# Kernel tuning notes

Measured on AMD Instinct MI355X. Metric: run time of the kernel, lower is better.

Reference implementation:

```python
import jax, jax.numpy as jnp
import numpy as np

H, DH, DM = 8, 128, 1024          # n_head, d_head, d_model (n_head*d_head == d_model)
SLEN, BSZ = 256, 64               # slen <= 256 forced by pi0[:, :l]
SCALE = 1.0 / DH ** 0.5
LN_EPS = 1e-5


def setup_inputs() -> dict:
    key = jax.random.key(0)
    k0, k1, k2, k3 = jax.random.split(key, 4)
    h = jax.random.normal(k0, (SLEN, BSZ, DM), jnp.float32)
    W_qkv = jax.random.normal(k1, (H * 4 * DH, DM), jnp.float32) * (DM ** -0.5)
    W_o = jax.random.normal(k2, (DM, H * DH), jnp.float32) * ((H * DH) ** -0.5)
    pi0 = jax.random.uniform(k3, (H, 256), jnp.float32)
    ln_gamma = jnp.ones((DM,), jnp.float32)
    ln_beta = jnp.zeros((DM,), jnp.float32)
    return {"h": h, "W_qkv": W_qkv, "W_o": W_o, "pi0": pi0,
            "ln_gamma": ln_gamma, "ln_beta": ln_beta}


def _phi(x):
    # elu(x)+1 feature map, then L1-normalize over the feature dim
    x = jax.nn.elu(x) + 1.0
    return x / jnp.sum(x, axis=-1, keepdims=True)


def _causal_linear_attn(q, k, v):
    # fast_weight_sum: out_t = sum_{s<=t} (q_t . k_s) v_s  (zero initial fast weights)
    # q,k,v: [b,h,l,d]
    l = q.shape[2]
    scores = jnp.einsum('bhld,bhsd->bhls', q, k)
    mask = jnp.tril(jnp.ones((l, l), dtype=bool))
    scores = jnp.where(mask, scores, jnp.zeros((), scores.dtype))
    return jnp.einsum('bhls,bhsd->bhld', scores, v)


def reference(h, W_qkv, W_o, pi0, ln_gamma, ln_beta):
    l, b, _ = h.shape
    # qkv projection: [l,b,H,4*DH] -> q, k1, k2, v (update_mode='rbf2keys')
    qkv = jnp.einsum('lbm,nm->lbn', h, W_qkv).reshape(l, b, H, 4 * DH)
    q, k1, k2, v = jnp.split(qkv, 4, axis=-1)
    # permute to [b, H, l, d]
    q = _phi(jnp.transpose(q, (1, 2, 0, 3)))
    k1 = _phi(jnp.transpose(k1, (1, 2, 0, 3)))
    k2 = _phi(jnp.transpose(k2, (1, 2, 0, 3)))
    v = jnp.transpose(v, (1, 2, 0, 3))
    # two fast-weight sums (skip_attn_normalization=True path)
    lo1 = _causal_linear_attn(q, k1, v)
    lo2 = _causal_linear_attn(q, k2, v)
    pi = jnp.clip(pi0, 0.0, 1.0)[None, :, :l, None]          # [1,H,l,1]
    layer_out = SCALE * (lo1 * pi + lo2 * (1.0 - pi))         # [b,H,l,d]
    # [b,H,l,d] -> [l,b,H*d]
    layer_out = jnp.transpose(layer_out, (2, 0, 1, 3)).reshape(l, b, H * DH)
    attn_out = jnp.einsum('lbn,mn->lbm', layer_out, W_o)
    # post-LN residual (pre_lnorm=False, dropout=0)
    x = h + attn_out
    mu = jnp.mean(x, axis=-1, keepdims=True)
    var = jnp.mean((x - mu) ** 2, axis=-1, keepdims=True)
    return ln_gamma * (x - mu) / jnp.sqrt(var + LN_EPS) + ln_beta
```

## Files before the change

### kernel.cpp

```cpp
#include <hip/hip_runtime.h>

#define H_     8
#define DM_    1024
#define NQKV_  4096
#define ROWS_  16384
#define PAIRS_ 512
#define SCALE_ 0.08838834764831845f
#define LN_EPS_ 1e-5f

typedef __attribute__((ext_vector_type(8))) short short8;
typedef __attribute__((ext_vector_type(4))) short short4v;
typedef __attribute__((ext_vector_type(4))) float floatx4;

__device__ __forceinline__ float b2f(unsigned short u) {
  union { unsigned int i; float f; } v; v.i = ((unsigned int)u) << 16; return v.f;
}
__device__ __forceinline__ unsigned short f2b(float f) {
  union { unsigned int i; float f; } v; v.f = f;
  unsigned int b = v.i;
  b += 0x7FFFu + ((b >> 16) & 1u);
  return (unsigned short)(b >> 16);
}

__device__ __forceinline__ void stage_async(const unsigned short* __restrict__ g,
                                            size_t ld, unsigned short* s, int tid) {
#pragma unroll
  for (int p = 0; p < 4; ++p) {
    int idx = p * 256 + tid;
    int r = idx >> 3, j = idx & 7;
    int cg = j ^ (r & 7);
    __builtin_amdgcn_global_load_lds(
        (const __attribute__((address_space(1))) unsigned int*)(g + (size_t)r * ld + cg * 8),
        (__attribute__((address_space(3))) unsigned int*)(s + (size_t)idx * 8),
        16, 0, 0);
  }
}
__device__ __forceinline__ void stage_h(const unsigned short* __restrict__ g,
                                        size_t o0, size_t o1,
                                        unsigned short* s, int lo0, int lo1) {
  __builtin_amdgcn_global_load_lds(
      (const __attribute__((address_space(1))) unsigned int*)(g + o0),
      (__attribute__((address_space(3))) unsigned int*)(s + lo0), 16, 0, 0);
  __builtin_amdgcn_global_load_lds(
      (const __attribute__((address_space(1))) unsigned int*)(g + o1),
      (__attribute__((address_space(3))) unsigned int*)(s + lo1), 16, 0, 0);
}
__device__ __forceinline__ short8 lds_frag(const unsigned short* s, int row, int cg) {
  return *(const short8*)(s + row * 64 + ((cg ^ (row & 7)) << 3));
}

__global__ __launch_bounds__(256) void cvt_all(const float* __restrict__ h,
                                               const float* __restrict__ wq,
                                               const float* __restrict__ wo,
                                               unsigned short* __restrict__ hb,
                                               unsigned short* __restrict__ wqb,
                                               unsigned short* __restrict__ wob) {
  int i = blockIdx.x * 256 + threadIdx.x;
  const float* src; unsigned short* dst; int off;
  if (i < 2097152)      { src = h;  dst = hb;  off = i; }
  else if (i < 2621440) { src = wq; dst = wqb; off = i - 2097152; }
  else                  { src = wo; dst = wob; off = i - 2621440; }
  const float4* s4 = (const float4*)(src + (size_t)off * 8);
  float4 v0 = s4[0], v1 = s4[1];
  union { short8 v; unsigned short u[8]; } pk;
  pk.u[0] = f2b(v0.x); pk.u[1] = f2b(v0.y); pk.u[2] = f2b(v0.z); pk.u[3] = f2b(v0.w);
  pk.u[4] = f2b(v1.x); pk.u[5] = f2b(v1.y); pk.u[6] = f2b(v1.z); pk.u[7] = f2b(v1.w);
  *(short8*)(dst + (size_t)off * 8) = pk.v;
}

#define TILE_BODY(T, BUF, OBUF)                                                \
  {                                                                            \
    unsigned short* SB = (BUF) + 16384;                                        \
    const unsigned short* aA0 = (BUF) + (wm * 128 + l16) * 64 + ((quad ^ s7) << 3); \
    const unsigned short* aA1 = (BUF) + (wm * 128 + l16) * 64 + (((4 + quad) ^ s7) << 3); \
    const unsigned short* bA0 = SB + (wn * 64 + l16) * 64 + ((quad ^ s7) << 3);\
    const unsigned short* bA1 = SB + (wn * 64 + l16) * 64 + (((4 + quad) ^ s7) << 3); \
    short8 a[8], b[4];                                                         \
                   \
    if ((T) < 15) {                                                            \
      size_t kn = (size_t)((T) + 1) * 64;                                      \
      stage_h(BbP + kn,  oB0, oB1, (OBUF) + 16384, lo0, lo1);                  \
      stage_h(BbHP + kn, oB0, oB1, (OBUF) + 24576, lo0, lo1);                  \
    }                                                                          \
    _Pragma("unroll")                                                          \
    for (int mt = 0; mt < 4; ++mt) {                                           \
      a[mt * 2 + 0] = *(const short8*)(aA0 + mt * 1024);                       \
      a[mt * 2 + 1] = *(const short8*)(aA1 + mt * 1024);                       \
    }                                                                          \
    _Pragma("unroll")                                                          \
    for (int nt = 0; nt < 2; ++nt) {                                           \
      b[nt * 2 + 0] = *(const short8*)(bA0 + nt * 1024);                       \
      b[nt * 2 + 1] = *(const short8*)(bA1 + nt * 1024);                       \
    }                                                                          \
    __builtin_amdgcn_sched_barrier(0);                                         \
    __builtin_amdgcn_s_barrier();                                              \
    __builtin_amdgcn_s_setprio(1);                                             \
    _Pragma("unroll")                                                          \
    for (int kk = 0; kk < 2; ++kk)                                             \
      _Pragma("unroll")                                                        \
      for (int m = 0; m < 4; ++m)                                              \
        _Pragma("unroll")                                                      \
        for (int n = 0; n < 2; ++n)                                            \
          acc[m][n] = __builtin_amdgcn_mfma_f32_16x16x32_bf16(a[m * 2 + kk], b[n * 2 + kk], acc[m][n], 0, 0, 0); \
    __builtin_amdgcn_s_setprio(0);                                             \
    __builtin_amdgcn_s_barrier();                                              \
                                                 \
    _Pragma("unroll")                                                          \
    for (int nt = 0; nt < 2; ++nt) {                                           \
      b[nt * 2 + 0] = *(const short8*)(bA0 + 2048 + nt * 1024);                \
      b[nt * 2 + 1] = *(const short8*)(bA1 + 2048 + nt * 1024);                \
    }                                                                          \
    __builtin_amdgcn_sched_barrier(0);                                         \
    __builtin_amdgcn_s_barrier();                                              \
    __builtin_amdgcn_s_setprio(1);                                             \
    _Pragma("unroll")                                                          \
    for (int kk = 0; kk < 2; ++kk)                                             \
      _Pragma("unroll")                                                        \
      for (int m = 0; m < 4; ++m)                                              \
        _Pragma("unroll")                                                      \
        for (int n = 0; n < 2; ++n)                                            \
          acc[m][2 + n] = __builtin_amdgcn_mfma_f32_16x16x32_bf16(a[m * 2 + kk], b[n * 2 + kk], acc[m][2 + n], 0, 0, 0); \
    __builtin_amdgcn_s_setprio(0);                                             \
    __builtin_amdgcn_s_barrier();                                              \
                                       \
    _Pragma("unroll")                                                          \
    for (int mt = 0; mt < 4; ++mt) {                                           \
      a[mt * 2 + 0] = *(const short8*)(aA0 + 4096 + mt * 1024);                \
      a[mt * 2 + 1] = *(const short8*)(aA1 + 4096 + mt * 1024);                \
    }                                                                          \
    __builtin_amdgcn_sched_barrier(0);                                         \
    __builtin_amdgcn_s_barrier();                                              \
    __builtin_amdgcn_s_setprio(1);                                             \
    _Pragma("unroll")                                                          \
    for (int kk = 0; kk < 2; ++kk)                                             \
      _Pragma("unroll")                                                        \
      for (int m = 0; m < 4; ++m)                                              \
        _Pragma("unroll")                                                      \
        for (int n = 0; n < 2; ++n)                                            \
          acc[4 + m][2 + n] = __builtin_amdgcn_mfma_f32_16x16x32_bf16(a[m * 2 + kk], b[n * 2 + kk], acc[4 + m][2 + n], 0, 0, 0); \
    __builtin_amdgcn_s_setprio(0);                                             \
    __builtin_amdgcn_s_barrier();                                              \
                \
    if ((T) < 14) {                                                            \
      size_t kt2 = (size_t)((T) + 2) * 64;                                     \
      stage_h(AbP + kt2,  oA0, oA1, (BUF),        lo0, lo1);                   \
      stage_h(AbHP + kt2, oA0, oA1, (BUF) + 8192, lo0, lo1);                   \
    }                                                                          \
    _Pragma("unroll")                                                          \
    for (int nt = 0; nt < 2; ++nt) {                                           \
      b[nt * 2 + 0] = *(const short8*)(bA0 + nt * 1024);                       \
      b[nt * 2 + 1] = *(const short8*)(bA1 + nt * 1024);                       \
    }                                                                          \
    __builtin_amdgcn_sched_barrier(0);                                         \
    __builtin_amdgcn_s_barrier();                                              \
    __builtin_amdgcn_s_setprio(1);                                             \
    _Pragma("unroll")                                                          \
    for (int kk = 0; kk < 2; ++kk)                                             \
      _Pragma("unroll")                                                        \
      for (int m = 0; m < 4; ++m)                                              \
        _Pragma("unroll")                                                      \
        for (int n = 0; n < 2; ++n)                                            \
          acc[4 + m][n] = __builtin_amdgcn_mfma_f32_16x16x32_bf16(a[m * 2 + kk], b[n * 2 + kk], acc[4 + m][n], 0, 0, 0); \
    __builtin_amdgcn_s_setprio(0);                                             \
    if ((T) < 14) { asm volatile("s_waitcnt vmcnt(4)" ::: "memory"); }         \
    else          { asm volatile("s_waitcnt vmcnt(0)" ::: "memory"); }         \
    __builtin_amdgcn_s_barrier();                                              \
  }

__global__ __launch_bounds__(512, 1) void qkv_gemm(const unsigned short* __restrict__ A,
                                                   const unsigned short* __restrict__ B,
                                                   unsigned short* __restrict__ QKV) {
  __shared__ alignas(16) unsigned short Sh[65536];
  int tid = threadIdx.x;
  int lane = tid & 63, wid = tid >> 6;
  int wm = wid >> 2, wn = wid & 3;
  int quad = lane >> 4, l16 = lane & 15;
  int s7 = l16 & 7;

  int bid = blockIdx.y * 16 + blockIdx.x;
  int swz = (bid & 7) * 128 + (bid >> 3);
  int bx = swz & 15, by = swz >> 4;
  int n0 = bx * 256, hh = bx >> 1, part0 = (bx & 1) * 2, bb = by;

  const unsigned short* AbP = A + (size_t)bb * DM_;
  const size_t lda = (size_t)64 * DM_;
  const unsigned short* AbHP = AbP + (size_t)128 * lda;
  const unsigned short* BbP = B + (size_t)n0 * DM_;
  const unsigned short* BbHP = BbP + (size_t)128 * DM_;

  int r0 = tid >> 3, jj = tid & 7;
  int cg = jj ^ (r0 & 7);
  size_t oA0 = (size_t)r0 * lda + cg * 8;
  size_t oA1 = (size_t)(r0 + 64) * lda + cg * 8;
  size_t oB0 = (size_t)r0 * DM_ + cg * 8;
  size_t oB1 = (size_t)(r0 + 64) * DM_ + cg * 8;
  int lo0 = tid * 8, lo1 = 4096 + tid * 8;

  floatx4 acc[8][4];
#pragma unroll
  for (int i = 0; i < 8; ++i)
#pragma unroll
    for (int j = 0; j < 4; ++j)
#pragma unroll
      for (int r = 0; r < 4; ++r) acc[i][j][r] = 0.f;

  stage_h(AbP,        oA0, oA1, Sh,         lo0, lo1);
  stage_h(AbHP,       oA0, oA1, Sh + 8192,  lo0, lo1);
  stage_h(BbP,        oB0, oB1, Sh + 16384, lo0, lo1);
  stage_h(BbHP,       oB0, oB1, Sh + 24576, lo0, lo1);
  stage_h(AbP + 64,   oA0, oA1, Sh + 32768, lo0, lo1);
  stage_h(AbHP + 64,  oA0, oA1, Sh + 40960, lo0, lo1);
  asm volatile("s_waitcnt vmcnt(4)" ::: "memory");
  __builtin_amdgcn_s_barrier();

  for (int t = 0; t < 16; t += 2) {
    TILE_BODY(t,     Sh,         Sh + 32768)
    TILE_BODY(t + 1, Sh + 32768, Sh)
  }

  __syncthreads();
  bool isV = (part0 + (wn >> 1)) == 3;
  float* Pf = (float*)Sh;
  float rsum[8][4];
  float inv[8][4];
  if (!isV) {
#pragma unroll
    for (int mt = 0; mt < 8; ++mt)
#pragma unroll
      for (int r = 0; r < 4; ++r) rsum[mt][r] = 0.f;
#pragma unroll
    for (int mt = 0; mt < 8; ++mt)
#pragma unroll
      for (int nt = 0; nt < 4; ++nt)
#pragma unroll
        for (int r = 0; r < 4; ++r) {
          float x = acc[mt][nt][r];
          float f = x > 0.f ? x + 1.f : __expf(x);
          acc[mt][nt][r] = f;
          rsum[mt][r] += f;
        }
#pragma unroll
    for (int off = 1; off < 16; off <<= 1)
#pragma unroll
      for (int mt = 0; mt < 8; ++mt)
#pragma unroll
        for (int r = 0; r < 4; ++r)
          rsum[mt][r] += __shfl_xor(rsum[mt][r], off);
    if (l16 == 0) {
#pragma unroll
      for (int mt = 0; mt < 8; ++mt)
#pragma unroll
        for (int r = 0; r < 4; ++r)
          Pf[(wm * 128 + mt * 16 + quad * 4 + r) * 4 + wn] = rsum[mt][r];
    }
  }
  __syncthreads();
  if (!isV) {
#pragma unroll
    for (int mt = 0; mt < 8; ++mt)
#pragma unroll
      for (int r = 0; r < 4; ++r)
        inv[mt][r] = 1.f / (rsum[mt][r] + Pf[(wm * 128 + mt * 16 + quad * 4 + r) * 4 + (wn ^ 1)]);
  }
  __syncthreads();

#pragma unroll
  for (int hq = 0; hq < 2; ++hq) {
    int part = part0 + hq;
    if ((wn >> 1) == hq) {
      if (part < 3) {
#pragma unroll
        for (int mt = 0; mt < 8; ++mt)
#pragma unroll
          for (int nt = 0; nt < 4; ++nt)
#pragma unroll
            for (int r = 0; r < 4; ++r) {
              int row = wm * 128 + mt * 16 + quad * 4 + r;
              int col = (wn & 1) * 64 + nt * 16 + l16;
              Sh[row * 136 + col] = f2b(acc[mt][nt][r] * inv[mt][r]);
            }
      } else {
#pragma unroll
        for (int mt = 0; mt < 8; ++mt)
#pragma unroll
          for (int nt = 0; nt < 4; ++nt)
#pragma unroll
            for (int r = 0; r < 4; ++r) {
              int d = (wn & 1) * 64 + nt * 16 + l16;
              int l = wm * 128 + mt * 16 + quad * 4 + r;
              Sh[d * 264 + l] = f2b(acc[mt][nt][r]);
            }
      }
    }
    __syncthreads();
    if (part < 3) {
      unsigned short* P = QKV + (size_t)part * 16777216 + (size_t)(bb * 8 + hh) * 32768;
      int c = tid & 15, g = tid >> 4;
#pragma unroll
      for (int j = 0; j < 8; ++j) {
        int row = j * 32 + g;
        *(short8*)(P + (size_t)row * 128 + c * 8) = *(const short8*)(Sh + row * 136 + c * 8);
      }
    } else {
      unsigned short* Vt = QKV + (size_t)3 * 16777216 + (size_t)(bb * 8 + hh) * 32768;
      int cg2 = tid & 31, g = tid >> 5;
#pragma unroll
      for (int j = 0; j < 8; ++j) {
        int d = j * 16 + g;
        *(short8*)(Vt + (size_t)d * 256 + cg2 * 8) = *(const short8*)(Sh + d * 264 + cg2 * 8);
      }
    }
    __syncthreads();
  }
}

__global__ __launch_bounds__(256) void scores_kernel(const unsigned short* __restrict__ QKV,
                                                     const float* __restrict__ pi0,
                                                     unsigned short* __restrict__ S) {
  __shared__ alignas(16) unsigned short Sh[24576];
  __shared__ float pis[128];
  unsigned short* As  = Sh;
  unsigned short* Bs1 = Sh + 8192;
  unsigned short* Bs2 = Sh + 16384;
  int p = blockIdx.z;
  int hh = p & 7;
  int tid = threadIdx.x;
  int lane = tid & 63, wid = tid >> 6;
  int wm = wid >> 1, wn = wid & 1;
  int quad = lane >> 4, l16 = lane & 15;
  int tix = blockIdx.x;
  int m0 = (tix >= 1) ? 128 : 0;
  int n0 = (tix == 2) ? 128 : 0;
  if (tid < 128) {
    float pv = pi0[hh * 256 + m0 + tid];
    pis[tid] = fminf(fmaxf(pv, 0.f), 1.f);
  }
  const unsigned short* Qb  = QKV + (size_t)p * 32768 + (size_t)m0 * 128;
  const unsigned short* K1b = QKV + 16777216     + (size_t)p * 32768 + (size_t)n0 * 128;
  const unsigned short* K2b = QKV + 2 * 16777216 + (size_t)p * 32768 + (size_t)n0 * 128;

  floatx4 acc1[4][4], acc2[4][4];
#pragma unroll
  for (int i = 0; i < 4; ++i)
#pragma unroll
    for (int j = 0; j < 4; ++j)
#pragma unroll
      for (int r = 0; r < 4; ++r) { acc1[i][j][r] = 0.f; acc2[i][j][r] = 0.f; }

  for (int kt = 0; kt < 128; kt += 64) {
    stage_async(Qb + kt, 128, As, tid);
    stage_async(K1b + kt, 128, Bs1, tid);
    stage_async(K2b + kt, 128, Bs2, tid);
    __syncthreads();
#pragma unroll
    for (int kk = 0; kk < 2; ++kk) {
      short8 af[4], b1[4], b2v[4];
#pragma unroll
      for (int mt = 0; mt < 4; ++mt)
        af[mt] = lds_frag(As, wm * 64 + mt * 16 + l16, kk * 4 + quad);
#pragma unroll
      for (int nt = 0; nt < 4; ++nt) {
        b1[nt]  = lds_frag(Bs1, wn * 64 + nt * 16 + l16, kk * 4 + quad);
        b2v[nt] = lds_frag(Bs2, wn * 64 + nt * 16 + l16, kk * 4 + quad);
      }
#pragma unroll
      for (int mt = 0; mt < 4; ++mt)
#pragma unroll
        for (int nt = 0; nt < 4; ++nt) {
          acc1[mt][nt] = __builtin_amdgcn_mfma_f32_16x16x32_bf16(af[mt], b1[nt],  acc1[mt][nt], 0, 0, 0);
          acc2[mt][nt] = __builtin_amdgcn_mfma_f32_16x16x32_bf16(af[mt], b2v[nt], acc2[mt][nt], 0, 0, 0);
        }
    }
    __syncthreads();
  }
#pragma unroll
  for (int mt = 0; mt < 4; ++mt)
#pragma unroll
    for (int nt = 0; nt < 4; ++nt)
#pragma unroll
      for (int r = 0; r < 4; ++r) {
        int tl = wm * 64 + mt * 16 + quad * 4 + r;
        int sl = wn * 64 + nt * 16 + l16;
        float pv = pis[tl];
        float v = (n0 + sl <= m0 + tl) ? (pv * acc1[mt][nt][r] + (1.f - pv) * acc2[mt][nt][r]) : 0.f;
        Sh[tl * 136 + sl] = f2b(v);
      }
  __syncthreads();
  int c = tid & 15, g = tid >> 4;
#pragma unroll
  for (int j = 0; j < 8; ++j) {
    int r = j * 16 + g;
    size_t gb = (size_t)p * 65536 + (size_t)(m0 + r) * 256 + n0 + c * 8;
    *(short8*)(S + gb) = *(const short8*)(Sh + r * 136 + c * 8);
  }
}

__global__ __launch_bounds__(256, 4) void pv_kernel(const unsigned short* __restrict__ S,
                                                    const unsigned short* __restrict__ Vt,
                                                    unsigned short* __restrict__ LO) {
  __shared__ alignas(16) unsigned short Sh[17408];
  unsigned short* As = Sh;
  unsigned short* Bs = Sh + 8192;
  int p = blockIdx.z;
  int b = p >> 3, hh = p & 7;
  int tid = threadIdx.x;
  int lane = tid & 63, wid = tid >> 6;
  int wm = wid >> 1, wn = wid & 1;
  int quad = lane >> 4, l16 = lane & 15;
  int m0 = blockIdx.y * 128;
  int kEnd = (blockIdx.y == 0) ? 128 : 256;
  const unsigned short* Ab = S  + (size_t)p * 65536 + (size_t)m0 * 256;
  const unsigned short* Bb = Vt + (size_t)p * 32768;

  floatx4 acc[4][4];
#pragma unroll
  for (int i = 0; i < 4; ++i)
#pragma unroll
    for (int j = 0; j < 4; ++j)
#pragma unroll
      for (int r = 0; r < 4; ++r) acc[i][j][r] = 0.f;

  for (int kt = 0; kt < kEnd; kt += 64) {
    stage_async(Ab + kt, 256, As, tid);
    stage_async(Bb + kt, 256, Bs, tid);
    __syncthreads();
#pragma unroll
    for (int kk = 0; kk < 2; ++kk) {
      short8 af[4], bfv[4];
#pragma unroll
      for (int mt = 0; mt < 4; ++mt)
        af[mt] = lds_frag(As, wm * 64 + mt * 16 + l16, kk * 4 + quad);
#pragma unroll
      for (int nt = 0; nt < 4; ++nt)
        bfv[nt] = lds_frag(Bs, wn * 64 + nt * 16 + l16, kk * 4 + quad);
#pragma unroll
      for (int mt = 0; mt < 4; ++mt)
#pragma unroll
        for (int nt = 0; nt < 4; ++nt)
          acc[mt][nt] = __builtin_amdgcn_mfma_f32_16x16x32_bf16(af[mt], bfv[nt], acc[mt][nt], 0, 0, 0);
    }
    __syncthreads();
  }
#pragma unroll
  for (int mt = 0; mt < 4; ++mt)
#pragma unroll
    for (int nt = 0; nt < 4; ++nt)
#pragma unroll
      for (int r = 0; r < 4; ++r) {
        int tl = wm * 64 + mt * 16 + quad * 4 + r;
        int d = wn * 64 + nt * 16 + l16;
        Sh[tl * 136 + d] = f2b(SCALE_ * acc[mt][nt][r]);
      }
  __syncthreads();
  int c = tid & 15, g = tid >> 4;
#pragma unroll
  for (int j = 0; j < 8; ++j) {
    int r = j * 16 + g;
    int t = m0 + r;
    size_t gb = ((size_t)t * 64 + b) * 1024 + hh * 128 + c * 8;
    *(short8*)(LO + gb) = *(const short8*)(Sh + r * 136 + c * 8);
  }
}

__global__ __launch_bounds__(512, 1) void wo_gemm(const unsigned short* __restrict__ A,
                                                  const unsigned short* __restrict__ B,
                                                  unsigned short* __restrict__ attn) {
  __shared__ alignas(16) unsigned short Sh[65536];
  int tid = threadIdx.x;
  int lane = tid & 63, wid = tid >> 6;
  int wm = wid >> 2, wn = wid & 3;
  int quad = lane >> 4, l16 = lane & 15;
  int s7 = l16 & 7;

  int bid = blockIdx.y * 4 + blockIdx.x;
  int swz = (bid & 7) * 32 + (bid >> 3);
  int bx = swz & 3, by = swz >> 2;
  int n0 = bx * 256, m0 = by * 256;

  const unsigned short* AbP = A + (size_t)m0 * DM_;
  const unsigned short* AbHP = AbP + (size_t)128 * DM_;
  const unsigned short* BbP = B + (size_t)n0 * DM_;
  const unsigned short* BbHP = BbP + (size_t)128 * DM_;

  int r0 = tid >> 3, jj = tid & 7;
  int cg = jj ^ (r0 & 7);
  size_t oA0 = (size_t)r0 * DM_ + cg * 8;
  size_t oA1 = (size_t)(r0 + 64) * DM_ + cg * 8;
  size_t oB0 = oA0, oB1 = oA1;
  int lo0 = tid * 8, lo1 = 4096 + tid * 8;

  floatx4 acc[8][4];
#pragma unroll
  for (int i = 0; i < 8; ++i)
#pragma unroll
    for (int j = 0; j < 4; ++j)
#pragma unroll
      for (int r = 0; r < 4; ++r) acc[i][j][r] = 0.f;

  stage_h(AbP,        oA0, oA1, Sh,         lo0, lo1);
  stage_h(AbHP,       oA0, oA1, Sh + 8192,  lo0, lo1);
  stage_h(BbP,        oB0, oB1, Sh + 16384, lo0, lo1);
  stage_h(BbHP,       oB0, oB1, Sh + 24576, lo0, lo1);
  stage_h(AbP + 64,   oA0, oA1, Sh + 32768, lo0, lo1);
  stage_h(AbHP + 64,  oA0, oA1, Sh + 40960, lo0, lo1);
  asm volatile("s_waitcnt vmcnt(4)" ::: "memory");
  __builtin_amdgcn_s_barrier();

  for (int t = 0; t < 16; t += 2) {
    TILE_BODY(t,     Sh,         Sh + 32768)
    TILE_BODY(t + 1, Sh + 32768, Sh)
  }

  __syncthreads();
#pragma unroll
  for (int hq = 0; hq < 2; ++hq) {
    if ((wn >> 1) == hq) {
#pragma unroll
      for (int mt = 0; mt < 8; ++mt)
#pragma unroll
        for (int nt = 0; nt < 4; ++nt)
#pragma unroll
          for (int r = 0; r < 4; ++r) {
            int row = wm * 128 + mt * 16 + quad * 4 + r;
            int col = (wn & 1) * 64 + nt * 16 + l16;
            Sh[row * 136 + col] = f2b(acc[mt][nt][r]);
          }
    }
    __syncthreads();
    int c = tid & 15, g = tid >> 4;
#pragma unroll
    for (int j = 0; j < 8; ++j) {
      int row = j * 32 + g;
      *(short8*)(attn + (size_t)(m0 + row) * DM_ + n0 + hq * 128 + c * 8) =
          *(const short8*)(Sh + row * 136 + c * 8);
    }
    __syncthreads();
  }
}

__global__ __launch_bounds__(256) void ln_res(const unsigned short* __restrict__ attn,
                                              const float* __restrict__ hin,
                                              const float* __restrict__ gamma,
                                              const float* __restrict__ beta,
                                              float* __restrict__ out) {
  int row = blockIdx.x;
  int tid = threadIdx.x;
  const unsigned short* ap = attn + (size_t)row * DM_ + tid * 4;
  const float* hp = hin + (size_t)row * DM_ + tid * 4;
  short4v av = *(const short4v*)ap;
  float4 hv = *(const float4*)hp;
  float x[4];
  x[0] = hv.x + b2f((unsigned short)av[0]);
  x[1] = hv.y + b2f((unsigned short)av[1]);
  x[2] = hv.z + b2f((unsigned short)av[2]);
  x[3] = hv.w + b2f((unsigned short)av[3]);
  float s  = x[0] + x[1] + x[2] + x[3];
  float ss = x[0] * x[0] + x[1] * x[1] + x[2] * x[2] + x[3] * x[3];
#pragma unroll
  for (int off = 32; off; off >>= 1) {
    s  += __shfl_down(s, off);
    ss += __shfl_down(ss, off);
  }
  __shared__ float rs[4], rss[4];
  int wv = tid >> 6, lane = tid & 63;
  if (lane == 0) { rs[wv] = s; rss[wv] = ss; }
  __syncthreads();
  float St  = rs[0] + rs[1] + rs[2] + rs[3];
  float SSt = rss[0] + rss[1] + rss[2] + rss[3];
  float mu = St * (1.f / DM_);
  float var = SSt * (1.f / DM_) - mu * mu;
  float rstd = rsqrtf(var + LN_EPS_);
  float4 o;
#pragma unroll
  for (int j = 0; j < 4; ++j) {
    int c = tid * 4 + j;
    (&o.x)[j] = gamma[c] * (x[j] - mu) * rstd + beta[c];
  }
  *(float4*)(out + (size_t)row * DM_ + tid * 4) = o;
}

extern "C" void kernel_launch(void* const* d_in, const int* in_sizes, int n_in,
                              void* d_out, int out_size, void* d_ws, size_t ws_size,
                              hipStream_t stream) {
  const float* h     = (const float*)d_in[0];
  const float* Wqkv  = (const float*)d_in[1];
  const float* Wo    = (const float*)d_in[2];
  const float* pi0   = (const float*)d_in[3];
  const float* gamma = (const float*)d_in[4];
  const float* beta  = (const float*)d_in[5];
  char* ws = (char*)d_ws;

  unsigned short* QKV   = (unsigned short*)ws;
  unsigned short* Sbuf  = (unsigned short*)(ws + 134217728ull);
  unsigned short* hb    = (unsigned short*)(ws + 134217728ull);
  unsigned short* Wqkvb = (unsigned short*)(ws + 167772160ull);
  unsigned short* Wob   = (unsigned short*)(ws + 201326592ull);
  unsigned short* LO    = (unsigned short*)ws;
  unsigned short* attn  = (unsigned short*)(ws + 134217728ull);
  float* X = (float*)d_out;

  dim3 blk(256);
  cvt_all<<<dim3(10752), blk, 0, stream>>>(h, Wqkv, Wo, hb, Wqkvb, Wob);
  qkv_gemm<<<dim3(16, 64, 1), dim3(512), 0, stream>>>(hb, Wqkvb, QKV);
  scores_kernel<<<dim3(3, 1, PAIRS_), blk, 0, stream>>>(QKV, pi0, Sbuf);
  pv_kernel<<<dim3(1, 2, PAIRS_), blk, 0, stream>>>(Sbuf, QKV + (size_t)3 * 16777216, LO);
  wo_gemm<<<dim3(4, 64, 1), dim3(512), 0, stream>>>(LO, Wob, attn);
  ln_res<<<dim3(ROWS_, 1, 1), blk, 0, stream>>>(attn, h, gamma, beta, X);
}
```

Before: 423.9 us.

## Replace double-buffered QKV GEMM main loop with single-buffered load-compute-sync loop

Drops the ping-pong LDS double buffering and interleaved async prefetch in the QKV projection GEMM. Each K-step now waits for all loads, computes the full tile from one buffer, synchronizes, then issues the next tile's loads, and LDS shrinks to about 68 KB. This removes the per-quadrant barriers and setprio scheduling, but global loads no longer overlap MFMA work, so the loop is likely to stall on memory latency.

```diff
diff --git a/kernel.cpp b/kernel.cpp
--- a/kernel.cpp
+++ b/kernel.cpp
@@ -76,7 +76,6 @@
     const unsigned short* bA0 = SB + (wn * 64 + l16) * 64 + ((quad ^ s7) << 3);\
     const unsigned short* bA1 = SB + (wn * 64 + l16) * 64 + (((4 + quad) ^ s7) << 3); \
     short8 a[8], b[4];                                                         \
-                   \
     if ((T) < 15) {                                                            \
       size_t kn = (size_t)((T) + 1) * 64;                                      \
       stage_h(BbP + kn,  oB0, oB1, (OBUF) + 16384, lo0, lo1);                  \
@@ -104,7 +103,6 @@
           acc[m][n] = __builtin_amdgcn_mfma_f32_16x16x32_bf16(a[m * 2 + kk], b[n * 2 + kk], acc[m][n], 0, 0, 0); \
     __builtin_amdgcn_s_setprio(0);                                             \
     __builtin_amdgcn_s_barrier();                                              \
-                                                 \
     _Pragma("unroll")                                                          \
     for (int nt = 0; nt < 2; ++nt) {                                           \
       b[nt * 2 + 0] = *(const short8*)(bA0 + 2048 + nt * 1024);                \
@@ -122,7 +120,6 @@
           acc[m][2 + n] = __builtin_amdgcn_mfma_f32_16x16x32_bf16(a[m * 2 + kk], b[n * 2 + kk], acc[m][2 + n], 0, 0, 0); \
     __builtin_amdgcn_s_setprio(0);                                             \
     __builtin_amdgcn_s_barrier();                                              \
-                                       \
     _Pragma("unroll")                                                          \
     for (int mt = 0; mt < 4; ++mt) {                                           \
       a[mt * 2 + 0] = *(const short8*)(aA0 + 4096 + mt * 1024);                \
@@ -140,7 +137,6 @@
           acc[4 + m][2 + n] = __builtin_amdgcn_mfma_f32_16x16x32_bf16(a[m * 2 + kk], b[n * 2 + kk], acc[4 + m][2 + n], 0, 0, 0); \
     __builtin_amdgcn_s_setprio(0);                                             \
     __builtin_amdgcn_s_barrier();                                              \
-                \
     if ((T) < 14) {                                                            \
       size_t kt2 = (size_t)((T) + 2) * 64;                                     \
       stage_h(AbP + kt2,  oA0, oA1, (BUF),        lo0, lo1);                   \
@@ -170,7 +166,7 @@
 __global__ __launch_bounds__(512, 1) void qkv_gemm(const unsigned short* __restrict__ A,
                                                    const unsigned short* __restrict__ B,
                                                    unsigned short* __restrict__ QKV) {
-  __shared__ alignas(16) unsigned short Sh[65536];
+  __shared__ alignas(16) unsigned short Sh[34816];
   int tid = threadIdx.x;
   int lane = tid & 63, wid = tid >> 6;
   int wm = wid >> 2, wn = wid & 3;
@@ -204,18 +200,76 @@
 #pragma unroll
       for (int r = 0; r < 4; ++r) acc[i][j][r] = 0.f;
 
-  stage_h(AbP,        oA0, oA1, Sh,         lo0, lo1);
-  stage_h(AbHP,       oA0, oA1, Sh + 8192,  lo0, lo1);
-  stage_h(BbP,        oB0, oB1, Sh + 16384, lo0, lo1);
-  stage_h(BbHP,       oB0, oB1, Sh + 24576, lo0, lo1);
-  stage_h(AbP + 64,   oA0, oA1, Sh + 32768, lo0, lo1);
-  stage_h(AbHP + 64,  oA0, oA1, Sh + 40960, lo0, lo1);
-  asm volatile("s_waitcnt vmcnt(4)" ::: "memory");
-  __builtin_amdgcn_s_barrier();
-
-  for (int t = 0; t < 16; t += 2) {
-    TILE_BODY(t,     Sh,         Sh + 32768)
-    TILE_BODY(t + 1, Sh + 32768, Sh)
+  stage_h(AbP,  oA0, oA1, Sh,         lo0, lo1);
+  stage_h(AbHP, oA0, oA1, Sh + 8192,  lo0, lo1);
+  stage_h(BbP,  oB0, oB1, Sh + 16384, lo0, lo1);
+  stage_h(BbHP, oB0, oB1, Sh + 24576, lo0, lo1);
+
+  const unsigned short* aA0 = Sh + (wm * 128 + l16) * 64 + ((quad ^ s7) << 3);
+  const unsigned short* aA1 = Sh + (wm * 128 + l16) * 64 + (((4 + quad) ^ s7) << 3);
+  const unsigned short* bA0 = Sh + 16384 + (wn * 64 + l16) * 64 + ((quad ^ s7) << 3);
+  const unsigned short* bA1 = Sh + 16384 + (wn * 64 + l16) * 64 + (((4 + quad) ^ s7) << 3);
+
+  for (int t = 0; t < 16; ++t) {
+    asm volatile("s_waitcnt vmcnt(0)" ::: "memory");
+    __builtin_amdgcn_s_barrier();
+    short8 a[8], b[8];
+#pragma unroll
+    for (int mt = 0; mt < 4; ++mt) {
+      a[mt * 2 + 0] = *(const short8*)(aA0 + mt * 1024);
+      a[mt * 2 + 1] = *(const short8*)(aA1 + mt * 1024);
+    }
+#pragma unroll
+    for (int nt = 0; nt < 2; ++nt) {
+      b[nt * 2 + 0] = *(const short8*)(bA0 + nt * 1024);
+      b[nt * 2 + 1] = *(const short8*)(bA1 + nt * 1024);
+    }
+#pragma unroll
+    for (int kk = 0; kk < 2; ++kk)
+#pragma unroll
+      for (int m = 0; m < 4; ++m)
+#pragma unroll
+        for (int n = 0; n < 2; ++n)
+          acc[m][n] = __builtin_amdgcn_mfma_f32_16x16x32_bf16(a[m * 2 + kk], b[n * 2 + kk], acc[m][n], 0, 0, 0);
+#pragma unroll
+    for (int nt = 0; nt < 2; ++nt) {
+      b[4 + nt * 2 + 0] = *(const short8*)(bA0 + 2048 + nt * 1024);
+      b[4 + nt * 2 + 1] = *(const short8*)(bA1 + 2048 + nt * 1024);
+    }
+#pragma unroll
+    for (int kk = 0; kk < 2; ++kk)
+#pragma unroll
+      for (int m = 0; m < 4; ++m)
+#pragma unroll
+        for (int n = 0; n < 2; ++n)
+          acc[m][2 + n] = __builtin_amdgcn_mfma_f32_16x16x32_bf16(a[m * 2 + kk], b[4 + n * 2 + kk], acc[m][2 + n], 0, 0, 0);
+#pragma unroll
+    for (int mt = 0; mt < 4; ++mt) {
+      a[mt * 2 + 0] = *(const short8*)(aA0 + 4096 + mt * 1024);
+      a[mt * 2 + 1] = *(const short8*)(aA1 + 4096 + mt * 1024);
+    }
+#pragma unroll
+    for (int kk = 0; kk < 2; ++kk)
+#pragma unroll
+      for (int m = 0; m < 4; ++m)
+#pragma unroll
+        for (int n = 0; n < 2; ++n)
+          acc[4 + m][2 + n] = __builtin_amdgcn_mfma_f32_16x16x32_bf16(a[m * 2 + kk], b[4 + n * 2 + kk], acc[4 + m][2 + n], 0, 0, 0);
+#pragma unroll
+    for (int kk = 0; kk < 2; ++kk)
+#pragma unroll
+      for (int m = 0; m < 4; ++m)
+#pragma unroll
+        for (int n = 0; n < 2; ++n)
+          acc[4 + m][n] = __builtin_amdgcn_mfma_f32_16x16x32_bf16(a[m * 2 + kk], b[n * 2 + kk], acc[4 + m][n], 0, 0, 0);
+    __syncthreads();
+    if (t < 15) {
+      size_t kn = (size_t)(t + 1) * 64;
+      stage_h(AbP + kn,  oA0, oA1, Sh,         lo0, lo1);
+      stage_h(AbHP + kn, oA0, oA1, Sh + 8192,  lo0, lo1);
+      stage_h(BbP + kn,  oB0, oB1, Sh + 16384, lo0, lo1);
+      stage_h(BbHP + kn, oB0, oB1, Sh + 24576, lo0, lo1);
+    }
   }
 
   __syncthreads();
```

Measured after the change: 436.2 us. 2.9% more time.

## Shrink qkv_gemm tile to 256x128 for higher occupancy, single-buffered

Applied to the files above, without the earlier changes.

Replaces the 256x256-tile qkv GEMM, which used 128KB of shared memory, double buffering and one block per CU, with a 256x128 tile (one head part per block). The new kernel uses 48KB of shared memory and launch bounds allowing four blocks per CU, and launches twice as many blocks. It gives up explicit double buffering, waiting on loads before each k-step, and relies on multiple resident blocks to hide latency. The epilogue is simplified because each block now handles a single q/k/v part.

```diff
diff --git a/kernel.cpp b/kernel.cpp
--- a/kernel.cpp
+++ b/kernel.cpp
@@ -22,6 +22,12 @@
   return (unsigned short)(b >> 16);
 }
 
+__device__ __forceinline__ void gl_lds(const unsigned short* g, unsigned short* s) {
+  __builtin_amdgcn_global_load_lds(
+      (const __attribute__((address_space(1))) unsigned int*)g,
+      (__attribute__((address_space(3))) unsigned int*)s, 16, 0, 0);
+}
+
 __device__ __forceinline__ void stage_async(const unsigned short* __restrict__ g,
                                             size_t ld, unsigned short* s, int tid) {
 #pragma unroll
@@ -29,21 +35,14 @@
     int idx = p * 256 + tid;
     int r = idx >> 3, j = idx & 7;
     int cg = j ^ (r & 7);
-    __builtin_amdgcn_global_load_lds(
-        (const __attribute__((address_space(1))) unsigned int*)(g + (size_t)r * ld + cg * 8),
-        (__attribute__((address_space(3))) unsigned int*)(s + (size_t)idx * 8),
-        16, 0, 0);
+    gl_lds(g + (size_t)r * ld + cg * 8, s + (size_t)idx * 8);
   }
 }
 __device__ __forceinline__ void stage_h(const unsigned short* __restrict__ g,
                                         size_t o0, size_t o1,
                                         unsigned short* s, int lo0, int lo1) {
-  __builtin_amdgcn_global_load_lds(
-      (const __attribute__((address_space(1))) unsigned int*)(g + o0),
-      (__attribute__((address_space(3))) unsigned int*)(s + lo0), 16, 0, 0);
-  __builtin_amdgcn_global_load_lds(
-      (const __attribute__((address_space(1))) unsigned int*)(g + o1),
-      (__attribute__((address_space(3))) unsigned int*)(s + lo1), 16, 0, 0);
+  gl_lds(g + o0, s + lo0);
+  gl_lds(g + o1, s + lo1);
 }
 __device__ __forceinline__ short8 lds_frag(const unsigned short* s, int row, int cg) {
   return *(const short8*)(s + row * 64 + ((cg ^ (row & 7)) << 3));
@@ -68,6 +67,181 @@
   *(short8*)(dst + (size_t)off * 8) = pk.v;
 }
 
+__global__ __launch_bounds__(512, 4) void qkv_gemm(const unsigned short* __restrict__ A,
+                                                   const unsigned short* __restrict__ B,
+                                                   unsigned short* __restrict__ QKV) {
+  __shared__ alignas(16) unsigned short Sh[24576];
+  unsigned short* As = Sh;
+  unsigned short* Bs = Sh + 16384;
+  int tid = threadIdx.x;
+  int lane = tid & 63, wid = tid >> 6;
+  int wm = wid >> 1, wn = wid & 1;
+  int quad = lane >> 4, l16 = lane & 15;
+  int s7 = l16 & 7;
+
+  int bid = blockIdx.y * 32 + blockIdx.x;
+  int swz = (bid & 7) * 256 + (bid >> 3);
+  int bx = swz & 31, by = swz >> 5;
+  int n0 = bx * 128, hh = bx >> 2, part = bx & 3, bb = by;
+
+  const unsigned short* AbP = A + (size_t)bb * DM_;
+  const size_t lda = (size_t)64 * DM_;
+  const unsigned short* BbP = B + (size_t)n0 * DM_;
+
+  int r0 = tid >> 3, jj = tid & 7;
+  int cg = jj ^ (r0 & 7);
+  size_t oA0 = (size_t)r0 * lda + cg * 8;
+  size_t oB0 = (size_t)r0 * DM_ + cg * 8;
+  int lo = tid * 8;
+
+  floatx4 acc[4][4];
+#pragma unroll
+  for (int i = 0; i < 4; ++i)
+#pragma unroll
+    for (int j = 0; j < 4; ++j)
+#pragma unroll
+      for (int r = 0; r < 4; ++r) acc[i][j][r] = 0.f;
+
+#pragma unroll
+  for (int p = 0; p < 4; ++p)
+    gl_lds(AbP + oA0 + (size_t)p * 64 * lda, As + lo + p * 4096);
+#pragma unroll
+  for (int p = 0; p < 2; ++p)
+    gl_lds(BbP + oB0 + (size_t)p * 64 * DM_, Bs + lo + p * 4096);
+
+  const unsigned short* aB0 = As + (wm * 64 + l16) * 64 + ((quad ^ s7) << 3);
+  const unsigned short* aB1 = As + (wm * 64 + l16) * 64 + (((4 + quad) ^ s7) << 3);
+  const unsigned short* bB0 = Bs + (wn * 64 + l16) * 64 + ((quad ^ s7) << 3);
+  const unsigned short* bB1 = Bs + (wn * 64 + l16) * 64 + (((4 + quad) ^ s7) << 3);
+
+  for (int t = 0; t < 16; ++t) {
+    asm volatile("s_waitcnt vmcnt(0)" ::: "memory");
+    __builtin_amdgcn_s_barrier();
+    short8 a[4], b[4];
+#pragma unroll
+    for (int mt = 0; mt < 4; ++mt) a[mt] = *(const short8*)(aB0 + mt * 1024);
+#pragma unroll
+    for (int nt = 0; nt < 4; ++nt) b[nt] = *(const short8*)(bB0 + nt * 1024);
+#pragma unroll
+    for (int mt = 0; mt < 4; ++mt)
+#pragma unroll
+      for (int nt = 0; nt < 4; ++nt)
+        acc[mt][nt] = __builtin_amdgcn_mfma_f32_16x16x32_bf16(a[mt], b[nt], acc[mt][nt], 0, 0, 0);
+#pragma unroll
+    for (int mt = 0; mt < 4; ++mt) a[mt] = *(const short8*)(aB1 + mt * 1024);
+#pragma unroll
+    for (int nt = 0; nt < 4; ++nt) b[nt] = *(const short8*)(bB1 + nt * 1024);
+#pragma unroll
+    for (int mt = 0; mt < 4; ++mt)
+#pragma unroll
+      for (int nt = 0; nt < 4; ++nt)
+        acc[mt][nt] = __builtin_amdgcn_mfma_f32_16x16x32_bf16(a[mt], b[nt], acc[mt][nt], 0, 0, 0);
+    __syncthreads();
+    if (t < 15) {
+      size_t kn = (size_t)(t + 1) * 64;
+#pragma unroll
+      for (int p = 0; p < 4; ++p)
+        gl_lds(AbP + kn + oA0 + (size_t)p * 64 * lda, As + lo + p * 4096);
+#pragma unroll
+      for (int p = 0; p < 2; ++p)
+        gl_lds(BbP + kn + oB0 + (size_t)p * 64 * DM_, Bs + lo + p * 4096);
+    }
+  }
+
+  __syncthreads();
+  int c = tid & 15, g = tid >> 4;
+  if (part < 3) {
+    float rsum[4][4];
+#pragma unroll
+    for (int mt = 0; mt < 4; ++mt)
+#pragma unroll
+      for (int r = 0; r < 4; ++r) rsum[mt][r] = 0.f;
+#pragma unroll
+    for (int mt = 0; mt < 4; ++mt)
+#pragma unroll
+      for (int nt = 0; nt < 4; ++nt)
+#pragma unroll
+        for (int r = 0; r < 4; ++r) {
+          float x = acc[mt][nt][r];
+          float f = x > 0.f ? x + 1.f : __expf(x);
+          acc[mt][nt][r] = f;
+          rsum[mt][r] += f;
+        }
+#pragma unroll
+    for (int off = 1; off < 16; off <<= 1)
+#pragma unroll
+      for (int mt = 0; mt < 4; ++mt)
+#pragma unroll
+        for (int r = 0; r < 4; ++r)
+          rsum[mt][r] += __shfl_xor(rsum[mt][r], off);
+    float* Pf = (float*)Sh;
+    if (l16 == 0) {
+#pragma unroll
+      for (int mt = 0; mt < 4; ++mt)
+#pragma unroll
+        for (int r = 0; r < 4; ++r)
+          Pf[(wm * 64 + mt * 16 + quad * 4 + r) * 2 + wn] = rsum[mt][r];
+    }
+    __syncthreads();
+    float inv[4][4];
+#pragma unroll
+    for (int mt = 0; mt < 4; ++mt)
+#pragma unroll
+      for (int r = 0; r < 4; ++r)
+        inv[mt][r] = 1.f / (rsum[mt][r] + Pf[(wm * 64 + mt * 16 + quad * 4 + r) * 2 + (wn ^ 1)]);
+    __syncthreads();
+    unsigned short* P = QKV + (size_t)part * 16777216 + (size_t)(bb * 8 + hh) * 32768;
+#pragma unroll
+    for (int hf = 0; hf < 2; ++hf) {
+      if ((wm >> 1) == hf) {
+#pragma unroll
+        for (int mt = 0; mt < 4; ++mt)
+#pragma unroll
+          for (int nt = 0; nt < 4; ++nt)
+#pragma unroll
+            for (int r = 0; r < 4; ++r) {
+              int row = (wm & 1) * 64 + mt * 16 + quad * 4 + r;
+              int col = wn * 64 + nt * 16 + l16;
+              Sh[row * 136 + col] = f2b(acc[mt][nt][r] * inv[mt][r]);
+            }
+      }
+      __syncthreads();
+#pragma unroll
+      for (int j = 0; j < 4; ++j) {
+        int row = j * 32 + g;
+        *(short8*)(P + (size_t)(hf * 128 + row) * 128 + c * 8) =
+            *(const short8*)(Sh + row * 136 + c * 8);
+      }
+      __syncthreads();
+    }
+  } else {
+    unsigned short* Vt = QKV + (size_t)3 * 16777216 + (size_t)(bb * 8 + hh) * 32768;
+#pragma unroll
+    for (int hf = 0; hf < 2; ++hf) {
+      if ((wm >> 1) == hf) {
+#pragma unroll
+        for (int mt = 0; mt < 4; ++mt)
+#pragma unroll
+          for (int nt = 0; nt < 4; ++nt)
+#pragma unroll
+            for (int r = 0; r < 4; ++r) {
+              int d = wn * 64 + nt * 16 + l16;
+              int l = (wm & 1) * 64 + mt * 16 + quad * 4 + r;
+              Sh[d * 136 + l] = f2b(acc[mt][nt][r]);
+            }
+      }
+      __syncthreads();
+#pragma unroll
+      for (int j = 0; j < 4; ++j) {
+        int d = j * 32 + g;
+        *(short8*)(Vt + (size_t)d * 256 + hf * 128 + c * 8) =
+            *(const short8*)(Sh + d * 136 + c * 8);
+      }
+      __syncthreads();
+    }
+  }
+}
+
 #define TILE_BODY(T, BUF, OBUF)                                                \
   {                                                                            \
     unsigned short* SB = (BUF) + 16384;                                        \
@@ -76,7 +250,6 @@
     const unsigned short* bA0 = SB + (wn * 64 + l16) * 64 + ((quad ^ s7) << 3);\
     const unsigned short* bA1 = SB + (wn * 64 + l16) * 64 + (((4 + quad) ^ s7) << 3); \
     short8 a[8], b[4];                                                         \
-                   \
     if ((T) < 15) {                                                            \
       size_t kn = (size_t)((T) + 1) * 64;                                      \
       stage_h(BbP + kn,  oB0, oB1, (OBUF) + 16384, lo0, lo1);                  \
@@ -104,7 +277,6 @@
           acc[m][n] = __builtin_amdgcn_mfma_f32_16x16x32_bf16(a[m * 2 + kk], b[n * 2 + kk], acc[m][n], 0, 0, 0); \
     __builtin_amdgcn_s_setprio(0);                                             \
     __builtin_amdgcn_s_barrier();                                              \
-                                                 \
     _Pragma("unroll")                                                          \
     for (int nt = 0; nt < 2; ++nt) {                                           \
       b[nt * 2 + 0] = *(const short8*)(bA0 + 2048 + nt * 1024);                \
@@ -122,7 +294,6 @@
           acc[m][2 + n] = __builtin_amdgcn_mfma_f32_16x16x32_bf16(a[m * 2 + kk], b[n * 2 + kk], acc[m][2 + n], 0, 0, 0); \
     __builtin_amdgcn_s_setprio(0);                                             \
     __builtin_amdgcn_s_barrier();                                              \
-                                       \
     _Pragma("unroll")                                                          \
     for (int mt = 0; mt < 4; ++mt) {                                           \
       a[mt * 2 + 0] = *(const short8*)(aA0 + 4096 + mt * 1024);                \
@@ -140,7 +311,6 @@
           acc[4 + m][2 + n] = __builtin_amdgcn_mfma_f32_16x16x32_bf16(a[m * 2 + kk], b[n * 2 + kk], acc[4 + m][2 + n], 0, 0, 0); \
     __builtin_amdgcn_s_setprio(0);                                             \
     __builtin_amdgcn_s_barrier();                                              \
-                \
     if ((T) < 14) {                                                            \
       size_t kt2 = (size_t)((T) + 2) * 64;                                     \
       stage_h(AbP + kt2,  oA0, oA1, (BUF),        lo0, lo1);                   \
@@ -166,153 +336,6 @@
     else          { asm volatile("s_waitcnt vmcnt(0)" ::: "memory"); }         \
     __builtin_amdgcn_s_barrier();                                              \
   }
-
-__global__ __launch_bounds__(512, 1) void qkv_gemm(const unsigned short* __restrict__ A,
-                                                   const unsigned short* __restrict__ B,
-                                                   unsigned short* __restrict__ QKV) {
-  __shared__ alignas(16) unsigned short Sh[65536];
-  int tid = threadIdx.x;
-  int lane = tid & 63, wid = tid >> 6;
-  int wm = wid >> 2, wn = wid & 3;
-  int quad = lane >> 4, l16 = lane & 15;
-  int s7 = l16 & 7;
-
-  int bid = blockIdx.y * 16 + blockIdx.x;
-  int swz = (bid & 7) * 128 + (bid >> 3);
-  int bx = swz & 15, by = swz >> 4;
-  int n0 = bx * 256, hh = bx >> 1, part0 = (bx & 1) * 2, bb = by;
-
-  const unsigned short* AbP = A + (size_t)bb * DM_;
-  const size_t lda = (size_t)64 * DM_;
-  const unsigned short* AbHP = AbP + (size_t)128 * lda;
-  const unsigned short* BbP = B + (size_t)n0 * DM_;
-  const unsigned short* BbHP = BbP + (size_t)128 * DM_;
-
-  int r0 = tid >> 3, jj = tid & 7;
-  int cg = jj ^ (r0 & 7);
-  size_t oA0 = (size_t)r0 * lda + cg * 8;
-  size_t oA1 = (size_t)(r0 + 64) * lda + cg * 8;
-  size_t oB0 = (size_t)r0 * DM_ + cg * 8;
-  size_t oB1 = (size_t)(r0 + 64) * DM_ + cg * 8;
-  int lo0 = tid * 8, lo1 = 4096 + tid * 8;
-
-  floatx4 acc[8][4];
-#pragma unroll
-  for (int i = 0; i < 8; ++i)
-#pragma unroll
-    for (int j = 0; j < 4; ++j)
-#pragma unroll
-      for (int r = 0; r < 4; ++r) acc[i][j][r] = 0.f;
-
-  stage_h(AbP,        oA0, oA1, Sh,         lo0, lo1);
-  stage_h(AbHP,       oA0, oA1, Sh + 8192,  lo0, lo1);
-  stage_h(BbP,        oB0, oB1, Sh + 16384, lo0, lo1);
-  stage_h(BbHP,       oB0, oB1, Sh + 24576, lo0, lo1);
-  stage_h(AbP + 64,   oA0, oA1, Sh + 32768, lo0, lo1);
-  stage_h(AbHP + 64,  oA0, oA1, Sh + 40960, lo0, lo1);
-  asm volatile("s_waitcnt vmcnt(4)" ::: "memory");
-  __builtin_amdgcn_s_barrier();
-
-  for (int t = 0; t < 16; t += 2) {
-    TILE_BODY(t,     Sh,         Sh + 32768)
-    TILE_BODY(t + 1, Sh + 32768, Sh)
-  }
-
-  __syncthreads();
-  bool isV = (part0 + (wn >> 1)) == 3;
-  float* Pf = (float*)Sh;
-  float rsum[8][4];
-  float inv[8][4];
-  if (!isV) {
-#pragma unroll
-    for (int mt = 0; mt < 8; ++mt)
-#pragma unroll
-      for (int r = 0; r < 4; ++r) rsum[mt][r] = 0.f;
-#pragma unroll
-    for (int mt = 0; mt < 8; ++mt)
-#pragma unroll
-      for (int nt = 0; nt < 4; ++nt)
-#pragma unroll
-        for (int r = 0; r < 4; ++r) {
-          float x = acc[mt][nt][r];
-          float f = x > 0.f ? x + 1.f : __expf(x);
-          acc[mt][nt][r] = f;
-          rsum[mt][r] += f;
-        }
-#pragma unroll
-    for (int off = 1; off < 16; off <<= 1)
-#pragma unroll
-      for (int mt = 0; mt < 8; ++mt)
-#pragma unroll
-        for (int r = 0; r < 4; ++r)
-          rsum[mt][r] += __shfl_xor(rsum[mt][r], off);
-    if (l16 == 0) {
-#pragma unroll
-      for (int mt = 0; mt < 8; ++mt)
-#pragma unroll
-        for (int r = 0; r < 4; ++r)
-          Pf[(wm * 128 + mt * 16 + quad * 4 + r) * 4 + wn] = rsum[mt][r];
-    }
-  }
-  __syncthreads();
-  if (!isV) {
-#pragma unroll
-    for (int mt = 0; mt < 8; ++mt)
-#pragma unroll
-      for (int r = 0; r < 4; ++r)
-        inv[mt][r] = 1.f / (rsum[mt][r] + Pf[(wm * 128 + mt * 16 + quad * 4 + r) * 4 + (wn ^ 1)]);
-  }
-  __syncthreads();
-
-#pragma unroll
-  for (int hq = 0; hq < 2; ++hq) {
-    int part = part0 + hq;
-    if ((wn >> 1) == hq) {
-      if (part < 3) {
-#pragma unroll
-        for (int mt = 0; mt < 8; ++mt)
-#pragma unroll
-          for (int nt = 0; nt < 4; ++nt)
-#pragma unroll
-            for (int r = 0; r < 4; ++r) {
-              int row = wm * 128 + mt * 16 + quad * 4 + r;
-              int col = (wn & 1) * 64 + nt * 16 + l16;
-              Sh[row * 136 + col] = f2b(acc[mt][nt][r] * inv[mt][r]);
-            }
-      } else {
-#pragma unroll
-        for (int mt = 0; mt < 8; ++mt)
-#pragma unroll
-          for (int nt = 0; nt < 4; ++nt)
-#pragma unroll
-            for (int r = 0; r < 4; ++r) {
-              int d = (wn & 1) * 64 + nt * 16 + l16;
-              int l = wm * 128 + mt * 16 + quad * 4 + r;
-              Sh[d * 264 + l] = f2b(acc[mt][nt][r]);
-            }
-      }
-    }
-    __syncthreads();
-    if (part < 3) {
-      unsigned short* P = QKV + (size_t)part * 16777216 + (size_t)(bb * 8 + hh) * 32768;
-      int c = tid & 15, g = tid >> 4;
-#pragma unroll
-      for (int j = 0; j < 8; ++j) {
-        int row = j * 32 + g;
-        *(short8*)(P + (size_t)row * 128 + c * 8) = *(const short8*)(Sh + row * 136 + c * 8);
-      }
-    } else {
-      unsigned short* Vt = QKV + (size_t)3 * 16777216 + (size_t)(bb * 8 + hh) * 32768;
-      int cg2 = tid & 31, g = tid >> 5;
-#pragma unroll
-      for (int j = 0; j < 8; ++j) {
-        int d = j * 16 + g;
-        *(short8*)(Vt + (size_t)d * 256 + cg2 * 8) = *(const short8*)(Sh + d * 264 + cg2 * 8);
-      }
-    }
-    __syncthreads();
-  }
-}
 
 __global__ __launch_bounds__(256) void scores_kernel(const unsigned short* __restrict__ QKV,
                                                      const float* __restrict__ pi0,
@@ -601,7 +624,7 @@
 
   dim3 blk(256);
   cvt_all<<<dim3(10752), blk, 0, stream>>>(h, Wqkv, Wo, hb, Wqkvb, Wob);
-  qkv_gemm<<<dim3(16, 64, 1), dim3(512), 0, stream>>>(hb, Wqkvb, QKV);
+  qkv_gemm<<<dim3(32, 64, 1), dim3(512), 0, stream>>>(hb, Wqkvb, QKV);
   scores_kernel<<<dim3(3, 1, PAIRS_), blk, 0, stream>>>(QKV, pi0, Sbuf);
   pv_kernel<<<dim3(1, 2, PAIRS_), blk, 0, stream>>>(Sbuf, QKV + (size_t)3 * 16777216, LO);
   wo_gemm<<<dim3(4, 64, 1), dim3(512), 0, stream>>>(LO, Wob, attn);
```

Result: slower. 498.2 us (+17.5%).
